# Performance work log

Measured on AMD Instinct MI355X. Metric: run time of the kernel, lower is better.

## Reference

```python
import jax, jax.numpy as jnp
import numpy as np

N_NODES = 100000
N_EDGES = 3200000
IN_CH = 128
OUT_CH = 64


def gcn_conv(x, src, dst, W, b, n):
    """PyG GCNConv: out = D^{-1/2} (A+I) D^{-1/2} (x @ W) + b.
    src/dst already include self-loops. Aggregation at dst (source_to_target)."""
    deg = jax.ops.segment_sum(jnp.ones_like(dst, x.dtype), dst, num_segments=n)  # [N]
    dinv = jnp.where(deg > 0, jax.lax.rsqrt(deg), 0.0)
    norm = dinv[src] * dinv[dst]                     # [E+N]
    xw = x @ W                                       # [N, out] dense GEMM first (PyG order)
    msgs = xw[src] * norm[:, None]                   # gather + scale, [E+N, out]
    return jax.ops.segment_sum(msgs, dst, num_segments=n) + b


def setup_inputs() -> dict:
    key = jax.random.key(0)
    ks = jax.random.split(key, 6)
    x = jax.random.normal(ks[0], (N_NODES, IN_CH), dtype=jnp.float32)
    edge_index = jax.random.randint(ks[1], (2, N_EDGES), 0, N_NODES, dtype=jnp.int32)
    # Glorot-style init for GCNConv weights
    W1 = jax.random.normal(ks[2], (IN_CH, IN_CH), dtype=jnp.float32) * (1.0 / np.sqrt(IN_CH))
    b1 = jnp.zeros((IN_CH,), dtype=jnp.float32)
    W2 = jax.random.normal(ks[3], (IN_CH, OUT_CH), dtype=jnp.float32) * (1.0 / np.sqrt(IN_CH))
    b2 = jnp.zeros((OUT_CH,), dtype=jnp.float32)
    return {"x": x, "edge_index": edge_index, "W1": W1, "b1": b1, "W2": W2, "b2": b2}


def reference(x, edge_index, W1, b1, W2, b2):
    n = x.shape[0]
    loop = jnp.arange(n, dtype=edge_index.dtype)
    src = jnp.concatenate([edge_index[0], loop])  # add self-loops once; reused by both layers
    dst = jnp.concatenate([edge_index[1], loop])
    h = jax.nn.sigmoid(gcn_conv(x, src, dst, W1, b1, n))
    return jax.nn.sigmoid(gcn_conv(h, src, dst, W2, b2, n))
```

## Files before the change

kernel.cpp:

```cpp
#include <hip/hip_runtime.h>
#include <hip/hip_bf16.h>
#include <hip/hip_fp16.h>

#define IN_CH 128
#define NODES_PER_BUCKET 128
#define BUCKET_CAP 5120
#define EPB 8192

using f32x2 = __attribute__((ext_vector_type(2))) float;

__device__ __forceinline__ float sigmoidf_(float x) { return 1.0f / (1.0f + __expf(-x)); }
__device__ __forceinline__ __half2 u2h(unsigned u) { return __builtin_bit_cast(__half2, u); }
__device__ __forceinline__ unsigned packh2(float a, float b) {
    return __builtin_bit_cast(unsigned, __float22half2_rn(make_float2(a, b)));
}

#if __has_builtin(__builtin_amdgcn_cvt_pk_f32_fp8) && __has_builtin(__builtin_amdgcn_cvt_pk_fp8_f32)
#define FP8_HW 1
#else
#define FP8_HW 0
__device__ __forceinline__ unsigned fp8_enc1(float f) {
    unsigned short us = __builtin_bit_cast(unsigned short, __float2half(f));
    unsigned s = (us >> 8) & 0x80u;
    unsigned mag = us & 0x7fffu;
    if (mag < 0x2400u) return s;
    unsigned t = mag - 0x2000u;
    t += 0x3Fu + ((t >> 7) & 1u);
    unsigned r = t >> 7;
    if (r > 0x7Eu) r = 0x7Eu;
    return s | r;
}
__device__ __forceinline__ float fp8_dec1(unsigned v) {
    unsigned s = (v & 0x80u) << 8;
    unsigned m = v & 0x7Fu;
    unsigned h = m ? (((m << 7) + 0x2000u) | s) : s;
    return __half2float(__builtin_bit_cast(__half, (unsigned short)h));
}
#endif

__device__ __forceinline__ void acc16(float* a, uint4 v) {
#if FP8_HW
    f32x2 t;
    t = __builtin_amdgcn_cvt_pk_f32_fp8(v.x, false); a[0] += t[0];  a[1] += t[1];
    t = __builtin_amdgcn_cvt_pk_f32_fp8(v.x, true);  a[2] += t[0];  a[3] += t[1];
    t = __builtin_amdgcn_cvt_pk_f32_fp8(v.y, false); a[4] += t[0];  a[5] += t[1];
    t = __builtin_amdgcn_cvt_pk_f32_fp8(v.y, true);  a[6] += t[0];  a[7] += t[1];
    t = __builtin_amdgcn_cvt_pk_f32_fp8(v.z, false); a[8] += t[0];  a[9] += t[1];
    t = __builtin_amdgcn_cvt_pk_f32_fp8(v.z, true);  a[10] += t[0]; a[11] += t[1];
    t = __builtin_amdgcn_cvt_pk_f32_fp8(v.w, false); a[12] += t[0]; a[13] += t[1];
    t = __builtin_amdgcn_cvt_pk_f32_fp8(v.w, true);  a[14] += t[0]; a[15] += t[1];
#else
    unsigned d[4] = {v.x, v.y, v.z, v.w};
#pragma unroll
    for (int q = 0; q < 4; q++)
#pragma unroll
        for (int b = 0; b < 4; b++) a[q * 4 + b] += fp8_dec1((d[q] >> (8 * b)) & 0xffu);
#endif
}

__device__ __forceinline__ unsigned pack4fp8(float a, float b, float c, float d) {
#if FP8_HW
    unsigned r = 0;
    r = __builtin_amdgcn_cvt_pk_fp8_f32(a, b, r, false);
    r = __builtin_amdgcn_cvt_pk_fp8_f32(c, d, r, true);
    return r;
#else
    return fp8_enc1(a) | (fp8_enc1(b) << 8) | (fp8_enc1(c) << 16) | (fp8_enc1(d) << 24);
#endif
}

__global__ __launch_bounds__(256) void k_bucket_scatter(const int* __restrict__ src,
                                                        const int* __restrict__ dst, int E,
                                                        int* __restrict__ bucketCnt, int NB,
                                                        unsigned* __restrict__ pairBuf) {
    __shared__ int hist[1024];
    int tid = threadIdx.x;
    for (int t = tid; t < 1024; t += 256) hist[t] = 0;
    __syncthreads();
    int base = blockIdx.x * EPB;
    int end = min(base + EPB, E);
    int cnt4 = (end - base) >> 2;
    const int4* d4 = (const int4*)(dst + base);
    const int4* s4 = (const int4*)(src + base);
    for (int i = tid; i < cnt4; i += 256) {
        int4 d = d4[i];
        atomicAdd(&hist[d.x >> 7], 1);
        atomicAdd(&hist[d.y >> 7], 1);
        atomicAdd(&hist[d.z >> 7], 1);
        atomicAdd(&hist[d.w >> 7], 1);
    }
    for (int i = base + (cnt4 << 2) + tid; i < end; i += 256)
        atomicAdd(&hist[dst[i] >> 7], 1);
    __syncthreads();
    for (int t = tid; t < NB; t += 256) {
        int c = hist[t];
        hist[t] = c ? atomicAdd(&bucketCnt[t], c) : 0;
    }
    __syncthreads();
    for (int i = tid; i < cnt4; i += 256) {
        int4 d = d4[i];
        int4 s = s4[i];
        int b, p;
        b = d.x >> 7; p = atomicAdd(&hist[b], 1);
        if (p < BUCKET_CAP) pairBuf[(size_t)b * BUCKET_CAP + p] = ((unsigned)s.x << 7) | (unsigned)(d.x & 127);
        b = d.y >> 7; p = atomicAdd(&hist[b], 1);
        if (p < BUCKET_CAP) pairBuf[(size_t)b * BUCKET_CAP + p] = ((unsigned)s.y << 7) | (unsigned)(d.y & 127);
        b = d.z >> 7; p = atomicAdd(&hist[b], 1);
        if (p < BUCKET_CAP) pairBuf[(size_t)b * BUCKET_CAP + p] = ((unsigned)s.z << 7) | (unsigned)(d.z & 127);
        b = d.w >> 7; p = atomicAdd(&hist[b], 1);
        if (p < BUCKET_CAP) pairBuf[(size_t)b * BUCKET_CAP + p] = ((unsigned)s.w << 7) | (unsigned)(d.w & 127);
    }
    for (int i = base + (cnt4 << 2) + tid; i < end; i += 256) {
        int d = dst[i];
        int b = d >> 7;
        int p = atomicAdd(&hist[b], 1);
        if (p < BUCKET_CAP) pairBuf[(size_t)b * BUCKET_CAP + p] = ((unsigned)src[i] << 7) | (unsigned)(d & 127);
    }
}

__global__ __launch_bounds__(1024) void k_scan_buckets(const int* __restrict__ bucketCnt, int NB,
                                                       int* __restrict__ bucketBase,
                                                       int* __restrict__ rowptr, int n) {
    __shared__ int sh[1024];
    int t = threadIdx.x;
    int v = (t < NB) ? min(bucketCnt[t], BUCKET_CAP) : 0;
    sh[t] = v;
    __syncthreads();
    for (int off = 1; off < 1024; off <<= 1) {
        int u = (t >= off) ? sh[t - off] : 0;
        __syncthreads();
        sh[t] += u;
        __syncthreads();
    }
    if (t < NB) bucketBase[t] = sh[t] - v;
    if (t == 1023) rowptr[n] = sh[1023];
}

__global__ __launch_bounds__(256) void k_bucket_place2(const unsigned* __restrict__ pairBuf,
                                                       const int* __restrict__ bucketCnt,
                                                       const int* __restrict__ bucketBase,
                                                       int* __restrict__ rowptr,
                                                       float* __restrict__ dinv,
                                                       int* __restrict__ col, int n) {
    __shared__ int hist[NODES_PER_BUCKET];
    __shared__ int excl[NODES_PER_BUCKET];
    __shared__ int stage[BUCKET_CAP];
    int b = blockIdx.x;
    int tid = threadIdx.x;
    int first = b * NODES_PER_BUCKET;
    if (tid < NODES_PER_BUCKET) hist[tid] = 0;
    __syncthreads();
    int cb = min(bucketCnt[b], BUCKET_CAP);
    const unsigned* p = pairBuf + (size_t)b * BUCKET_CAP;
    for (int e = tid; e < cb; e += 256) atomicAdd(&hist[p[e] & 127], 1);
    __syncthreads();
    int v = (tid < NODES_PER_BUCKET) ? hist[tid] : 0;
    if (tid < NODES_PER_BUCKET) excl[tid] = v;
    __syncthreads();
    for (int off = 1; off < NODES_PER_BUCKET; off <<= 1) {
        int u = (tid < NODES_PER_BUCKET && tid >= off) ? excl[tid - off] : 0;
        __syncthreads();
        if (tid < NODES_PER_BUCKET) excl[tid] += u;
        __syncthreads();
    }
    int base = bucketBase[b];
    if (tid < NODES_PER_BUCKET) {
        int node = first + tid;
        int ex = excl[tid] - v;
        if (node < n) {
            rowptr[node] = base + ex;
            dinv[node] = rsqrtf((float)(v + 1));
        }
        hist[tid] = ex;
    }
    __syncthreads();
    for (int e = tid; e < cb; e += 256) {
        unsigned pr = p[e];
        int lpos = atomicAdd(&hist[pr & 127], 1);
        stage[lpos] = (int)(pr >> 7);
    }
    __syncthreads();
    for (int i = tid; i < cb; i += 256) col[base + i] = stage[i];
}

template <int OUTC, bool INHALF>
__global__ __launch_bounds__(256) void k_gemm_scale(const void* __restrict__ Xv,
                                                    const float* __restrict__ W,
                                                    const float* __restrict__ dinv,
                                                    unsigned char* __restrict__ Yb, int n) {
    constexpr int TN = OUTC / 16;
    __shared__ float xs[16][65];
    __shared__ float ws[16 * OUTC];
    int tid = threadIdx.x;
    int row0 = blockIdx.x * 64;
    int tx = tid & 15;
    int ty = tid >> 4;

    float acc[4][TN];
#pragma unroll
    for (int i = 0; i < 4; i++)
#pragma unroll
        for (int j = 0; j < TN; j++) acc[i][j] = 0.0f;

    for (int k0 = 0; k0 < IN_CH; k0 += 16) {
        {
            int r = tid >> 2;
            int kq = (tid & 3) * 4;
            int grow = row0 + r;
            float4 xv = make_float4(0.f, 0.f, 0.f, 0.f);
            if (grow < n) {
                if constexpr (INHALF) {
                    uint2 xu = *(const uint2*)((const unsigned short*)Xv + (size_t)grow * IN_CH + k0 + kq);
                    __half2 p0 = u2h(xu.x), p1 = u2h(xu.y);
                    xv = make_float4(__low2float(p0), __high2float(p0), __low2float(p1), __high2float(p1));
                } else {
                    xv = *(const float4*)((const float*)Xv + (size_t)grow * IN_CH + k0 + kq);
                }
            }
            xs[kq + 0][r] = xv.x;
            xs[kq + 1][r] = xv.y;
            xs[kq + 2][r] = xv.z;
            xs[kq + 3][r] = xv.w;
        }
        {
            const float4* wsrc = (const float4*)(W + k0 * OUTC);
            float4* wdst = (float4*)ws;
#pragma unroll
            for (int j = 0; j < OUTC / 64; j++) wdst[tid + j * 256] = wsrc[tid + j * 256];
        }
        __syncthreads();
#pragma unroll
        for (int kk = 0; kk < 16; kk++) {
            float a[4];
            *(float4*)a = *(const float4*)&xs[kk][ty * 4];
            float bb[TN];
#pragma unroll
            for (int j = 0; j < TN / 4; j++)
                *(float4*)&bb[j * 4] = *(const float4*)&ws[kk * OUTC + tx * TN + j * 4];
#pragma unroll
            for (int i = 0; i < 4; i++)
#pragma unroll
                for (int j = 0; j < TN; j++) acc[i][j] = fmaf(a[i], bb[j], acc[i][j]);
        }
        __syncthreads();
    }
#pragma unroll
    for (int i = 0; i < 4; i++) {
        int grow = row0 + ty * 4 + i;
        if (grow < n) {
            float dvv = dinv[grow];
            if constexpr (TN == 8) {
                uint2 o;
                o.x = pack4fp8(acc[i][0] * dvv, acc[i][1] * dvv, acc[i][2] * dvv, acc[i][3] * dvv);
                o.y = pack4fp8(acc[i][4] * dvv, acc[i][5] * dvv, acc[i][6] * dvv, acc[i][7] * dvv);
                ((uint2*)(Yb + (size_t)grow * 128))[tx] = o;
            } else {
                unsigned o = pack4fp8(acc[i][0] * dvv, acc[i][1] * dvv, acc[i][2] * dvv, acc[i][3] * dvv);
                ((unsigned*)(Yb + (size_t)grow * 64))[tx] = o;
            }
        }
    }
}

template <int C, bool OUTHALF>
__global__ __launch_bounds__(256) void k_agg(const uint4* __restrict__ Y4,
                                             const int* __restrict__ rowptr,
                                             const int* __restrict__ col,
                                             const float* __restrict__ dinv,
                                             const float* __restrict__ bias,
                                             void* __restrict__ out, int n, int zidx) {
    constexpr int LPE = C / 16;
    constexpr int NPW = 64 / LPE;
    constexpr int RS = C / 16;
    int gid = blockIdx.x * blockDim.x + threadIdx.x;
    int wid = gid >> 6;
    int lane = gid & 63;
    int g = lane / LPE;
    int sub = lane % LPE;
    int node = wid * NPW + g;
    bool valid = node < n;
    int nc = valid ? node : 0;
    int s0 = rowptr[nc];
    int s1 = valid ? rowptr[nc + 1] : s0;

    float a0[16], a1[16];
#pragma unroll
    for (int k = 0; k < 16; k++) { a0[k] = 0.f; a1[k] = 0.f; }

    {
        int idx = valid ? node : zidx;
        uint4 v = Y4[(size_t)idx * RS + sub];
        acc16(a0, v);
    }
    int e = s0;
    for (; e + 4 <= s1; e += 4) {
        int c0 = col[e];
        int c1 = col[e + 1];
        int c2 = col[e + 2];
        int c3 = col[e + 3];
        uint4 v0 = Y4[(size_t)c0 * RS + sub];
        uint4 v1 = Y4[(size_t)c1 * RS + sub];
        uint4 v2 = Y4[(size_t)c2 * RS + sub];
        uint4 v3 = Y4[(size_t)c3 * RS + sub];
        acc16(a0, v0);
        acc16(a1, v1);
        acc16(a0, v2);
        acc16(a1, v3);
    }
    for (; e < s1; e++) {
        uint4 v = Y4[(size_t)col[e] * RS + sub];
        acc16(a0, v);
    }
#pragma unroll
    for (int k = 0; k < 16; k++) a0[k] += a1[k];

    if (valid) {
        float dv = dinv[node];
        float4 bv[4];
        bv[0] = *(const float4*)&bias[sub * 16];
        bv[1] = *(const float4*)&bias[sub * 16 + 4];
        bv[2] = *(const float4*)&bias[sub * 16 + 8];
        bv[3] = *(const float4*)&bias[sub * 16 + 12];
        float o[16];
#pragma unroll
        for (int q = 0; q < 4; q++) {
            const float* bq = (const float*)&bv[q];
#pragma unroll
            for (int b = 0; b < 4; b++) o[q * 4 + b] = sigmoidf_(a0[q * 4 + b] * dv + bq[b]);
        }
        if constexpr (OUTHALF) {
            constexpr int OR = C / 8;
            uint4 h0, h1;
            h0.x = packh2(o[0], o[1]);   h0.y = packh2(o[2], o[3]);
            h0.z = packh2(o[4], o[5]);   h0.w = packh2(o[6], o[7]);
            h1.x = packh2(o[8], o[9]);   h1.y = packh2(o[10], o[11]);
            h1.z = packh2(o[12], o[13]); h1.w = packh2(o[14], o[15]);
            ((uint4*)out)[(size_t)node * OR + sub * 2] = h0;
            ((uint4*)out)[(size_t)node * OR + sub * 2 + 1] = h1;
        } else {
            float* op = (float*)out + (size_t)node * C + sub * 16;
            *(float4*)(op + 0)  = make_float4(o[0], o[1], o[2], o[3]);
            *(float4*)(op + 4)  = make_float4(o[4], o[5], o[6], o[7]);
            *(float4*)(op + 8)  = make_float4(o[8], o[9], o[10], o[11]);
            *(float4*)(op + 12) = make_float4(o[12], o[13], o[14], o[15]);
        }
    }
}

extern "C" void kernel_launch(void* const* d_in, const int* in_sizes, int n_in,
                              void* d_out, int out_size, void* d_ws, size_t ws_size,
                              hipStream_t stream) {
    const float* x  = (const float*)d_in[0];
    const int* eidx = (const int*)d_in[1];
    const float* W1 = (const float*)d_in[2];
    const float* b1 = (const float*)d_in[3];
    const float* W2 = (const float*)d_in[4];
    const float* b2 = (const float*)d_in[5];
    float* out = (float*)d_out;

    int n = in_sizes[0] / IN_CH;
    int E = in_sizes[1] / 2;
    const int* srcv = eidx;
    const int* dstv = eidx + E;
    int NB = (n + NODES_PER_BUCKET - 1) / NODES_PER_BUCKET;

    char* w = (char*)d_ws;
    auto alloc = [&](size_t bytes) {
        char* p = w;
        w += (bytes + 255) & ~(size_t)255;
        return p;
    };
    int* bucketCnt      = (int*)alloc((size_t)NB * 4);
    int* bucketBase     = (int*)alloc((size_t)NB * 4);
    unsigned* pairBuf   = (unsigned*)alloc((size_t)NB * BUCKET_CAP * 4);
    int* rowptr         = (int*)alloc(((size_t)n + 1) * 4);
    float* dinv         = (float*)alloc((size_t)n * 4);
    int* col            = (int*)alloc((size_t)E * 4);
    unsigned char* y    = (unsigned char*)alloc(((size_t)n + 1) * 128);
    unsigned short* h   = (unsigned short*)alloc((size_t)n * IN_CH * 2);

    hipMemsetAsync(bucketCnt, 0, (size_t)NB * 4, stream);
    hipMemsetAsync(y + (size_t)n * 128, 0, 128, stream);

    int nblk = (E + EPB - 1) / EPB;
    k_bucket_scatter<<<nblk, 256, 0, stream>>>(srcv, dstv, E, bucketCnt, NB, pairBuf);
    k_scan_buckets<<<1, 1024, 0, stream>>>(bucketCnt, NB, bucketBase, rowptr, n);
    k_bucket_place2<<<NB, 256, 0, stream>>>(pairBuf, bucketCnt, bucketBase, rowptr, dinv, col, n);

    int gemmGrid = (n + 63) / 64;

    k_gemm_scale<128, false><<<gemmGrid, 256, 0, stream>>>(x, W1, dinv, y, n);
    k_agg<128, true><<<(n + 31) / 32, 256, 0, stream>>>((const uint4*)y, rowptr, col, dinv, b1, h, n, n);
    k_gemm_scale<64, true><<<gemmGrid, 256, 0, stream>>>(h, W2, dinv, y, n);
    k_agg<64, false><<<(n + 63) / 64, 256, 0, stream>>>((const uint4*)y, rowptr, col, dinv, b2, out, n, 2 * n);
}
```

Measured before the change: 259.7 us.

## Cache edge ranks in registers during bucket scatter; unroll gather loop by eight

The bucket scatter kernel now reads src/dst once. It records each edge's packed pair and its local rank from the histogram atomic in registers, then writes using the bucket base plus the rank. This removes the second pass over global memory and the second round of shared atomics. The SpMM gather loop is unrolled to eight independent row loads, and the tail is padded with zero-row indices so more loads are in flight at once. The cost is higher register pressure: 64 cached values per thread in the scatter and 8 uint4 loads in the gather.

```diff
diff --git a/kernel.cpp b/kernel.cpp
--- a/kernel.cpp
+++ b/kernel.cpp
@@ -79,42 +79,67 @@
     __syncthreads();
     int base = blockIdx.x * EPB;
     int end = min(base + EPB, E);
-    int cnt4 = (end - base) >> 2;
+    int cnt = end - base;
+    int cnt4 = cnt >> 2;
     const int4* d4 = (const int4*)(dst + base);
     const int4* s4 = (const int4*)(src + base);
-    for (int i = tid; i < cnt4; i += 256) {
-        int4 d = d4[i];
-        atomicAdd(&hist[d.x >> 7], 1);
-        atomicAdd(&hist[d.y >> 7], 1);
-        atomicAdd(&hist[d.z >> 7], 1);
-        atomicAdd(&hist[d.w >> 7], 1);
-    }
-    for (int i = base + (cnt4 << 2) + tid; i < end; i += 256)
-        atomicAdd(&hist[dst[i] >> 7], 1);
+
+    unsigned pr[8][4];
+    unsigned rkb[8][4];
+#pragma unroll
+    for (int j = 0; j < 8; j++) {
+        int i = tid + j * 256;
+        if (i < cnt4) {
+            int4 d = d4[i];
+            int4 s = s4[i];
+            int b, r;
+            b = d.x >> 7; r = atomicAdd(&hist[b], 1);
+            pr[j][0] = ((unsigned)s.x << 7) | (unsigned)(d.x & 127); rkb[j][0] = ((unsigned)r << 10) | (unsigned)b;
+            b = d.y >> 7; r = atomicAdd(&hist[b], 1);
+            pr[j][1] = ((unsigned)s.y << 7) | (unsigned)(d.y & 127); rkb[j][1] = ((unsigned)r << 10) | (unsigned)b;
+            b = d.z >> 7; r = atomicAdd(&hist[b], 1);
+            pr[j][2] = ((unsigned)s.z << 7) | (unsigned)(d.z & 127); rkb[j][2] = ((unsigned)r << 10) | (unsigned)b;
+            b = d.w >> 7; r = atomicAdd(&hist[b], 1);
+            pr[j][3] = ((unsigned)s.w << 7) | (unsigned)(d.w & 127); rkb[j][3] = ((unsigned)r << 10) | (unsigned)b;
+        }
+    }
+    unsigned prT = 0, rkbT = 0;
+    bool hasT = false;
+    {
+        int tl = cnt & 3;
+        if (tid < tl) {
+            int i = base + (cnt4 << 2) + tid;
+            int d = dst[i];
+            int b = d >> 7;
+            int r = atomicAdd(&hist[b], 1);
+            prT = ((unsigned)src[i] << 7) | (unsigned)(d & 127);
+            rkbT = ((unsigned)r << 10) | (unsigned)b;
+            hasT = true;
+        }
+    }
     __syncthreads();
     for (int t = tid; t < NB; t += 256) {
         int c = hist[t];
         hist[t] = c ? atomicAdd(&bucketCnt[t], c) : 0;
     }
     __syncthreads();
-    for (int i = tid; i < cnt4; i += 256) {
-        int4 d = d4[i];
-        int4 s = s4[i];
-        int b, p;
-        b = d.x >> 7; p = atomicAdd(&hist[b], 1);
-        if (p < BUCKET_CAP) pairBuf[(size_t)b * BUCKET_CAP + p] = ((unsigned)s.x << 7) | (unsigned)(d.x & 127);
-        b = d.y >> 7; p = atomicAdd(&hist[b], 1);
-        if (p < BUCKET_CAP) pairBuf[(size_t)b * BUCKET_CAP + p] = ((unsigned)s.y << 7) | (unsigned)(d.y & 127);
-        b = d.z >> 7; p = atomicAdd(&hist[b], 1);
-        if (p < BUCKET_CAP) pairBuf[(size_t)b * BUCKET_CAP + p] = ((unsigned)s.z << 7) | (unsigned)(d.z & 127);
-        b = d.w >> 7; p = atomicAdd(&hist[b], 1);
-        if (p < BUCKET_CAP) pairBuf[(size_t)b * BUCKET_CAP + p] = ((unsigned)s.w << 7) | (unsigned)(d.w & 127);
-    }
-    for (int i = base + (cnt4 << 2) + tid; i < end; i += 256) {
-        int d = dst[i];
-        int b = d >> 7;
-        int p = atomicAdd(&hist[b], 1);
-        if (p < BUCKET_CAP) pairBuf[(size_t)b * BUCKET_CAP + p] = ((unsigned)src[i] << 7) | (unsigned)(d & 127);
+#pragma unroll
+    for (int j = 0; j < 8; j++) {
+        int i = tid + j * 256;
+        if (i < cnt4) {
+#pragma unroll
+            for (int q = 0; q < 4; q++) {
+                unsigned t = rkb[j][q];
+                int b = (int)(t & 1023u);
+                int pos = hist[b] + (int)(t >> 10);
+                if (pos < BUCKET_CAP) pairBuf[(size_t)b * BUCKET_CAP + pos] = pr[j][q];
+            }
+        }
+    }
+    if (hasT) {
+        int b = (int)(rkbT & 1023u);
+        int pos = hist[b] + (int)(rkbT >> 10);
+        if (pos < BUCKET_CAP) pairBuf[(size_t)b * BUCKET_CAP + pos] = prT;
     }
 }
 
@@ -283,9 +308,9 @@
     int s0 = rowptr[nc];
     int s1 = valid ? rowptr[nc + 1] : s0;
 
-    float a0[16], a1[16];
-#pragma unroll
-    for (int k = 0; k < 16; k++) { a0[k] = 0.f; a1[k] = 0.f; }
+    float a0[16];
+#pragma unroll
+    for (int k = 0; k < 16; k++) a0[k] = 0.f;
 
     {
         int idx = valid ? node : zidx;
@@ -293,26 +318,62 @@
         acc16(a0, v);
     }
     int e = s0;
-    for (; e + 4 <= s1; e += 4) {
+    for (; e + 8 <= s1; e += 8) {
         int c0 = col[e];
         int c1 = col[e + 1];
         int c2 = col[e + 2];
         int c3 = col[e + 3];
+        int c4 = col[e + 4];
+        int c5 = col[e + 5];
+        int c6 = col[e + 6];
+        int c7 = col[e + 7];
         uint4 v0 = Y4[(size_t)c0 * RS + sub];
         uint4 v1 = Y4[(size_t)c1 * RS + sub];
         uint4 v2 = Y4[(size_t)c2 * RS + sub];
         uint4 v3 = Y4[(size_t)c3 * RS + sub];
+        uint4 v4 = Y4[(size_t)c4 * RS + sub];
+        uint4 v5 = Y4[(size_t)c5 * RS + sub];
+        uint4 v6 = Y4[(size_t)c6 * RS + sub];
+        uint4 v7 = Y4[(size_t)c7 * RS + sub];
         acc16(a0, v0);
-        acc16(a1, v1);
+        acc16(a0, v1);
         acc16(a0, v2);
-        acc16(a1, v3);
-    }
-    for (; e < s1; e++) {
-        uint4 v = Y4[(size_t)col[e] * RS + sub];
-        acc16(a0, v);
-    }
-#pragma unroll
-    for (int k = 0; k < 16; k++) a0[k] += a1[k];
+        acc16(a0, v3);
+        acc16(a0, v4);
+        acc16(a0, v5);
+        acc16(a0, v6);
+        acc16(a0, v7);
+    }
+    if (e < s1) {
+        int i0 = min(e + 0, s1 - 1), i1 = min(e + 1, s1 - 1);
+        int i2 = min(e + 2, s1 - 1), i3 = min(e + 3, s1 - 1);
+        int i4 = min(e + 4, s1 - 1), i5 = min(e + 5, s1 - 1);
+        int i6 = min(e + 6, s1 - 1), i7 = min(e + 7, s1 - 1);
+        int c0 = (e + 0 < s1) ? col[i0] : zidx;
+        int c1 = (e + 1 < s1) ? col[i1] : zidx;
+        int c2 = (e + 2 < s1) ? col[i2] : zidx;
+        int c3 = (e + 3 < s1) ? col[i3] : zidx;
+        int c4 = (e + 4 < s1) ? col[i4] : zidx;
+        int c5 = (e + 5 < s1) ? col[i5] : zidx;
+        int c6 = (e + 6 < s1) ? col[i6] : zidx;
+        int c7 = (e + 7 < s1) ? col[i7] : zidx;
+        uint4 v0 = Y4[(size_t)c0 * RS + sub];
+        uint4 v1 = Y4[(size_t)c1 * RS + sub];
+        uint4 v2 = Y4[(size_t)c2 * RS + sub];
+        uint4 v3 = Y4[(size_t)c3 * RS + sub];
+        uint4 v4 = Y4[(size_t)c4 * RS + sub];
+        uint4 v5 = Y4[(size_t)c5 * RS + sub];
+        uint4 v6 = Y4[(size_t)c6 * RS + sub];
+        uint4 v7 = Y4[(size_t)c7 * RS + sub];
+        acc16(a0, v0);
+        acc16(a0, v1);
+        acc16(a0, v2);
+        acc16(a0, v3);
+        acc16(a0, v4);
+        acc16(a0, v5);
+        acc16(a0, v6);
+        acc16(a0, v7);
+    }
 
     if (valid) {
         float dv = dinv[node];
```

Result: faster. 241.2 us (-7.1%).
